# Optimization experiments

Hardware: AMD Instinct MI355X
Metric: run time of the kernel (lower is better)

The kernel has to match this reference:

```python
import jax, jax.numpy as jnp
import numpy as np

NEG_SLOPE = 0.01  # F.leaky_relu default

def setup_inputs() -> dict:
    key = jax.random.key(0)
    ks = jax.random.split(key, 5)
    N, in_dim, out_dim = 8192, 256, 256
    x = jax.random.normal(ks[0], (N, in_dim), dtype=jnp.float32)
    W_fc = jax.random.normal(ks[1], (in_dim, out_dim), dtype=jnp.float32) / np.sqrt(in_dim)
    b_fc = jnp.zeros((out_dim,), dtype=jnp.float32)
    # attn_fc weight [2*out_dim] split into the two halves acting on h_i and h_j
    a1 = jax.random.normal(ks[2], (out_dim,), dtype=jnp.float32) / np.sqrt(2 * out_dim)
    a2 = jax.random.normal(ks[3], (out_dim,), dtype=jnp.float32) / np.sqrt(2 * out_dim)
    a_b = jnp.zeros((), dtype=jnp.float32)
    return {"x": x, "W_fc": W_fc, "b_fc": b_fc, "a1": a1, "a2": a2, "a_b": a_b}

def reference(x, W_fc, b_fc, a1, a2, a_b):
    # h = fc(x)
    h = x @ W_fc + b_fc                       # [N, out_dim]
    # attn_fc(cat[h_i, h_j]) == h_i.a1 + h_j.a2 + a_b (exact decomposition of the Linear)
    s1 = h @ a1                               # [N]
    s2 = h @ a2                               # [N]
    e = jax.nn.leaky_relu(s1[:, None] + s2[None, :] + a_b, NEG_SLOPE)  # [N, N]
    attention = jax.nn.softmax(e, axis=1)     # row-softmax over neighbors j
    return attention @ h                      # [N, out_dim]
```

## Files before the change

### kernel.cpp

```cpp
#include <hip/hip_runtime.h>
#include <math.h>


#define NN 8192
#define DD 256
#define NB 8192
#define CH 512
#define POS (NN / CH)
#define RANGE 8.0f
#define SCALE (NB / (2.0f * RANGE))
#define NEG_SLOPE 0.01f

__device__ __forceinline__ int bucket_of(float v) {
    v = fminf(fmaxf(v, -RANGE), RANGE);
    int b = (int)floorf((v + RANGE) * SCALE);
    if (b < 0) b = 0;
    if (b > NB - 1) b = NB - 1;
    return b;
}

__global__ __launch_bounds__(256) void ka_gemm(
    const float* __restrict__ x, const float* __restrict__ W,
    const float* __restrict__ bfc, const float* __restrict__ a1,
    const float* __restrict__ a2,
    float* __restrict__ h, float* __restrict__ s1, float* __restrict__ s2,
    float* __restrict__ E, float* __restrict__ F, int* __restrict__ cnt)
{
    const int t = threadIdx.x;
    const int ct = t & 63;
    const int rt = t >> 6;
    const int row0 = blockIdx.x * 16;
    __shared__ float xs[16][DD];

#pragma unroll
    for (int i = 0; i < 4; ++i) {
        const int f = i * 256 + t;
        const int r = f >> 6, c4 = f & 63;
        *reinterpret_cast<float4*>(&xs[r][c4 * 4]) =
            *reinterpret_cast<const float4*>(&x[(size_t)(row0 + r) * DD + c4 * 4]);
    }
    __syncthreads();

    float acc[4][4];
#pragma unroll
    for (int r = 0; r < 4; ++r)
#pragma unroll
        for (int c = 0; c < 4; ++c) acc[r][c] = 0.f;

#pragma unroll 2
    for (int k4 = 0; k4 < DD / 4; ++k4) {
        float4 wv[4];
#pragma unroll
        for (int kk = 0; kk < 4; ++kk)
            wv[kk] = *reinterpret_cast<const float4*>(&W[(size_t)(k4 * 4 + kk) * DD + ct * 4]);
        float4 xr[4];
#pragma unroll
        for (int r = 0; r < 4; ++r)
            xr[r] = *reinterpret_cast<const float4*>(&xs[rt * 4 + r][k4 * 4]);
#pragma unroll
        for (int kk = 0; kk < 4; ++kk) {
#pragma unroll
            for (int r = 0; r < 4; ++r) {
                const float xv = (kk == 0) ? xr[r].x : (kk == 1) ? xr[r].y : (kk == 2) ? xr[r].z : xr[r].w;
                acc[r][0] = fmaf(xv, wv[kk].x, acc[r][0]);
                acc[r][1] = fmaf(xv, wv[kk].y, acc[r][1]);
                acc[r][2] = fmaf(xv, wv[kk].z, acc[r][2]);
                acc[r][3] = fmaf(xv, wv[kk].w, acc[r][3]);
            }
        }
    }

    const float4 bv  = *reinterpret_cast<const float4*>(&bfc[ct * 4]);
    const float4 a1v = *reinterpret_cast<const float4*>(&a1[ct * 4]);
    const float4 a2v = *reinterpret_cast<const float4*>(&a2[ct * 4]);
    const int lane = t & 63;

#pragma unroll
    for (int r = 0; r < 4; ++r) {
        acc[r][0] += bv.x; acc[r][1] += bv.y; acc[r][2] += bv.z; acc[r][3] += bv.w;
        const int row = row0 + rt * 4 + r;
        float4 hv = make_float4(acc[r][0], acc[r][1], acc[r][2], acc[r][3]);
        *reinterpret_cast<float4*>(&h[(size_t)row * DD + ct * 4]) = hv;
        float v1 = acc[r][0] * a1v.x + acc[r][1] * a1v.y + acc[r][2] * a1v.z + acc[r][3] * a1v.w;
        float v2 = acc[r][0] * a2v.x + acc[r][1] * a2v.y + acc[r][2] * a2v.z + acc[r][3] * a2v.w;
#pragma unroll
        for (int off = 32; off; off >>= 1) {
            v1 += __shfl_xor(v1, off, 64);
            v2 += __shfl_xor(v2, off, 64);
        }
        if (lane == 0) {
            s1[row] = v1;
            s2[row] = v2;
            E[row] = expf(v2);
            F[row] = expf(NEG_SLOPE * v2);
            atomicAdd(&cnt[bucket_of(v2)], 1);
        }
    }
}

__global__ __launch_bounds__(256) void kb_scan(int* __restrict__ cnt, int* __restrict__ boff)
{
    __shared__ int lds[256];
    const int t = threadIdx.x;
    const int base = t * 32;
    int loc[32];
    int s = 0;
#pragma unroll
    for (int k = 0; k < 32; ++k) { loc[k] = s; s += cnt[base + k]; }
    lds[t] = s;
    __syncthreads();
    for (int off = 1; off < 256; off <<= 1) {
        const int v = (t >= off) ? lds[t - off] : 0;
        __syncthreads();
        lds[t] += v;
        __syncthreads();
    }
    const int excl = (t > 0) ? lds[t - 1] : 0;
#pragma unroll
    for (int k = 0; k < 32; ++k) {
        const int val = excl + loc[k];
        boff[base + k] = val;
        cnt[base + k] = val;
    }
    if (t == 0) boff[NB] = NN;
}

__global__ __launch_bounds__(256) void kc_scatter(
    const float* __restrict__ s2, int* __restrict__ cursor, int* __restrict__ perm)
{
    const int j = blockIdx.x * blockDim.x + threadIdx.x;
    if (j < NN) {
        const int b = bucket_of(s2[j]);
        const int p = atomicAdd(&cursor[b], 1);
        perm[p] = j;
    }
}

__global__ __launch_bounds__(256) void kd1_tot(
    const float* __restrict__ h, const float* __restrict__ E, const float* __restrict__ F,
    const int* __restrict__ perm,
    float* __restrict__ TE, float* __restrict__ TF,
    float* __restrict__ sTE, float* __restrict__ sTF)
{
    const int c = blockIdx.x;
    const int t = threadIdx.x;
    __shared__ int jj[POS];
    __shared__ float Ee[POS], Ff[POS];
    if (t < POS) {
        const int j = perm[c * POS + t];
        jj[t] = j; Ee[t] = E[j]; Ff[t] = F[j];
    }
    __syncthreads();
    float te = 0.f, tf = 0.f;
#pragma unroll
    for (int k = 0; k < POS; ++k) {
        const float hv = h[(size_t)jj[k] * DD + t];
        te = fmaf(Ee[k], hv, te);
        tf = fmaf(Ff[k], hv, tf);
    }
    TE[c * DD + t] = te;
    TF[c * DD + t] = tf;
    if (t == 0) {
        float se = 0.f, sf = 0.f;
#pragma unroll
        for (int k = 0; k < POS; ++k) { se += Ee[k]; sf += Ff[k]; }
        sTE[c] = se; sTF[c] = sf;
    }
}

__global__ __launch_bounds__(512) void kd2_scan(
    float* __restrict__ TE, float* __restrict__ TF,
    float* __restrict__ sTE, float* __restrict__ sTF,
    float* __restrict__ PSE, float* __restrict__ PSF,
    float* __restrict__ psE, float* __restrict__ psF)
{
    const int t = threadIdx.x;
    const int b = blockIdx.x;
    __shared__ float lds[CH];

    if (b < 512) {
        const bool isE = (b < 256);
        const int d = isE ? b : (b - 256);
        float* __restrict__ A = isE ? TE : TF;
        const float v = A[(size_t)t * DD + d];
        const int pos = isE ? (CH - 1 - t) : t;
        lds[pos] = v;
        __syncthreads();
        for (int off = 1; off < CH; off <<= 1) {
            const float add = (pos >= off) ? lds[pos - off] : 0.f;
            __syncthreads();
            lds[pos] += add;
            __syncthreads();
        }
        const float incl = lds[pos];
        A[(size_t)t * DD + d] = incl - v;
        if (t == 0) {
            if (isE) PSE[(size_t)NN * DD + d] = 0.f;
            else     PSF[(size_t)NN * DD + d] = lds[CH - 1];
        }
    } else {
        const float vE = sTE[t];
        const float vF = sTF[t];
        lds[CH - 1 - t] = vE;
        __syncthreads();
        for (int off = 1; off < CH; off <<= 1) {
            const int pos = CH - 1 - t;
            const float add = (pos >= off) ? lds[pos - off] : 0.f;
            __syncthreads();
            lds[pos] += add;
            __syncthreads();
        }
        const float inclE = lds[CH - 1 - t];
        __syncthreads();
        lds[t] = vF;
        __syncthreads();
        for (int off = 1; off < CH; off <<= 1) {
            const float add = (t >= off) ? lds[t - off] : 0.f;
            __syncthreads();
            lds[t] += add;
            __syncthreads();
        }
        const float inclF = lds[t];
        const float totF = lds[CH - 1];
        sTE[t] = inclE - vE;
        sTF[t] = inclF - vF;
        if (t == 0) { psE[NN] = 0.f; psF[NN] = totF; }
    }
}

__global__ __launch_bounds__(256) void kd3_write(
    const float* __restrict__ h, const float* __restrict__ E, const float* __restrict__ F,
    const int* __restrict__ perm,
    const float* __restrict__ TE, const float* __restrict__ TF,
    const float* __restrict__ sTE, const float* __restrict__ sTF,
    float* __restrict__ PSE, float* __restrict__ PSF,
    float* __restrict__ psE, float* __restrict__ psF)
{
    const int c = blockIdx.x;
    const int t = threadIdx.x;
    __shared__ int jj[POS];
    __shared__ float Ee[POS], Ff[POS];
    if (t < POS) {
        const int j = perm[c * POS + t];
        jj[t] = j; Ee[t] = E[j]; Ff[t] = F[j];
    }
    __syncthreads();
    const int p0 = c * POS;

    float runE = TE[c * DD + t];
#pragma unroll
    for (int k = POS - 1; k >= 0; --k) {
        runE = fmaf(Ee[k], h[(size_t)jj[k] * DD + t], runE);
        PSE[(size_t)(p0 + k) * DD + t] = runE;
    }
    float runF = TF[c * DD + t];
#pragma unroll
    for (int k = 0; k < POS; ++k) {
        PSF[(size_t)(p0 + k) * DD + t] = runF;
        runF = fmaf(Ff[k], h[(size_t)jj[k] * DD + t], runF);
    }
    if (t == 0) {
        float rE = sTE[c];
#pragma unroll
        for (int k = POS - 1; k >= 0; --k) { rE += Ee[k]; psE[p0 + k] = rE; }
        float rF = sTF[c];
#pragma unroll
        for (int k = 0; k < POS; ++k) { psF[p0 + k] = rF; rF += Ff[k]; }
    }
}

__global__ __launch_bounds__(256) void ke_out(
    const float* __restrict__ h, const float* __restrict__ s1, const float* __restrict__ s2,
    const float* __restrict__ E, const float* __restrict__ F,
    const int* __restrict__ perm, const int* __restrict__ boff,
    const float* __restrict__ PSE, const float* __restrict__ PSF,
    const float* __restrict__ psE, const float* __restrict__ psF,
    const float* __restrict__ ab, float* __restrict__ out)
{
    const int i = blockIdx.x;
    const int t = threadIdx.x;
    const float c = s1[i] + ab[0];
    const float tau = -c;
    const int Bt = bucket_of(tau);
    const float A = expf(c);
    const float Alo = expf(NEG_SLOPE * c);

    const int p0 = boff[Bt], p1 = boff[Bt + 1];
    float num = A * PSE[(size_t)p1 * DD + t] + Alo * PSF[(size_t)p0 * DD + t];
    float den = A * psE[p1] + Alo * psF[p0];

    for (int p = p0; p < p1; ++p) {
        const int j = perm[p];
        const float hv = h[(size_t)j * DD + t];
        if (s2[j] >= tau) {
            const float w = A * E[j];
            num = fmaf(w, hv, num);
            den += w;
        } else {
            const float w = Alo * F[j];
            num = fmaf(w, hv, num);
            den += w;
        }
    }
    out[(size_t)i * DD + t] = num / den;
}

extern "C" void kernel_launch(void* const* d_in, const int* in_sizes, int n_in,
                              void* d_out, int out_size, void* d_ws, size_t ws_size,
                              hipStream_t stream)
{
    const float* x   = (const float*)d_in[0];
    const float* W   = (const float*)d_in[1];
    const float* bfc = (const float*)d_in[2];
    const float* a1  = (const float*)d_in[3];
    const float* a2  = (const float*)d_in[4];
    const float* ab  = (const float*)d_in[5];
    float* out = (float*)d_out;

    float* h   = (float*)d_ws;
    float* PSE = h + (size_t)NN * DD;
    float* PSF = PSE + (size_t)(NN + 1) * DD;
    float* TE  = PSF + (size_t)(NN + 1) * DD;
    float* TF  = TE + (size_t)CH * DD;
    float* s1  = TF + (size_t)CH * DD;
    float* s2  = s1 + NN;
    float* E   = s2 + NN;
    float* F   = E + NN;
    float* psE = F + NN;
    float* psF = psE + (NN + 1);
    float* sTE = psF + (NN + 1);
    float* sTF = sTE + CH;
    int* cnt   = (int*)(sTF + CH);
    int* boff  = cnt + NB;
    int* perm  = boff + (NB + 1);

    hipMemsetAsync(cnt, 0, NB * sizeof(int), stream);
    ka_gemm<<<NN / 16, 256, 0, stream>>>(x, W, bfc, a1, a2, h, s1, s2, E, F, cnt);
    kb_scan<<<1, 256, 0, stream>>>(cnt, boff);
    kc_scatter<<<NN / 256, 256, 0, stream>>>(s2, cnt, perm);
    kd1_tot<<<CH, 256, 0, stream>>>(h, E, F, perm, TE, TF, sTE, sTF);
    kd2_scan<<<513, 512, 0, stream>>>(TE, TF, sTE, sTF, PSE, PSF, psE, psF);
    kd3_write<<<CH, 256, 0, stream>>>(h, E, F, perm, TE, TF, sTE, sTF, PSE, PSF, psE, psF);
    ke_out<<<NN, 256, 0, stream>>>(h, s1, s2, E, F, perm, boff, PSE, PSF, psE, psF, ab, out);
}
```

Before: 144.2 us.

## Fully sort scores and replace per-position prefix arrays with chunk prefixes plus binary search

Adds a rank pass that fully sorts s2 within each bucket, so every row can binary-search its exact threshold position. The full N×D per-position prefix arrays PSE/PSF and their write kernel are removed. Each output row now combines a chunk-level prefix with a partial 16-element chunk walk, which cuts large memory writes and reads. Kernels are also reshaped to one wave per chunk or row with float4 loads, and exp is recomputed on the fly instead of stored. The trade-off is extra sequential work in the rank kernel when buckets are large, plus a per-row binary search.

```diff
diff --git a/kernel.cpp b/kernel.cpp
--- a/kernel.cpp
+++ b/kernel.cpp
@@ -24,7 +24,7 @@
     const float* __restrict__ bfc, const float* __restrict__ a1,
     const float* __restrict__ a2,
     float* __restrict__ h, float* __restrict__ s1, float* __restrict__ s2,
-    float* __restrict__ E, float* __restrict__ F, int* __restrict__ cnt)
+    int* __restrict__ cnt)
 {
     const int t = threadIdx.x;
     const int ct = t & 63;
@@ -91,8 +91,6 @@
         if (lane == 0) {
             s1[row] = v1;
             s2[row] = v2;
-            E[row] = expf(v2);
-            F[row] = expf(NEG_SLOPE * v2);
             atomicAdd(&cnt[bucket_of(v2)], 1);
         }
     }
@@ -136,173 +134,182 @@
     }
 }
 
+__global__ __launch_bounds__(256) void kc2_rank(
+    const float* __restrict__ s2, const int* __restrict__ perm,
+    const int* __restrict__ boff, int* __restrict__ perm2, float* __restrict__ s2s)
+{
+    const int j = blockIdx.x * blockDim.x + threadIdx.x;
+    if (j < NN) {
+        const float v = s2[j];
+        const int bk = bucket_of(v);
+        const int p0 = boff[bk], p1 = boff[bk + 1];
+        int rank = 0;
+        for (int p = p0; p < p1; ++p) {
+            const int k = perm[p];
+            const float vk = s2[k];
+            rank += (vk < v) || (vk == v && k < j);
+        }
+        const int pos = p0 + rank;
+        perm2[pos] = j;
+        s2s[pos] = v;
+    }
+}
+
 __global__ __launch_bounds__(256) void kd1_tot(
-    const float* __restrict__ h, const float* __restrict__ E, const float* __restrict__ F,
-    const int* __restrict__ perm,
+    const float* __restrict__ h, const int* __restrict__ perm2,
+    const float* __restrict__ s2s,
     float* __restrict__ TE, float* __restrict__ TF,
     float* __restrict__ sTE, float* __restrict__ sTF)
 {
-    const int c = blockIdx.x;
-    const int t = threadIdx.x;
-    __shared__ int jj[POS];
-    __shared__ float Ee[POS], Ff[POS];
-    if (t < POS) {
-        const int j = perm[c * POS + t];
-        jj[t] = j; Ee[t] = E[j]; Ff[t] = F[j];
-    }
+    const int w = threadIdx.x >> 6, lane = threadIdx.x & 63;
+    const int c = blockIdx.x * 4 + w;
+    const int p0 = c * POS;
+    float vE[POS], vF[POS];
+    int jj[POS];
+#pragma unroll
+    for (int k = 0; k < POS; ++k) {
+        const float v = s2s[p0 + k];
+        vE[k] = expf(v);
+        vF[k] = expf(NEG_SLOPE * v);
+        jj[k] = perm2[p0 + k];
+    }
+    float4 te = make_float4(0.f, 0.f, 0.f, 0.f);
+    float4 tf = make_float4(0.f, 0.f, 0.f, 0.f);
+#pragma unroll
+    for (int k = 0; k < POS; ++k) {
+        const float4 hv = *reinterpret_cast<const float4*>(&h[(size_t)jj[k] * DD + lane * 4]);
+        te.x = fmaf(vE[k], hv.x, te.x); te.y = fmaf(vE[k], hv.y, te.y);
+        te.z = fmaf(vE[k], hv.z, te.z); te.w = fmaf(vE[k], hv.w, te.w);
+        tf.x = fmaf(vF[k], hv.x, tf.x); tf.y = fmaf(vF[k], hv.y, tf.y);
+        tf.z = fmaf(vF[k], hv.z, tf.z); tf.w = fmaf(vF[k], hv.w, tf.w);
+    }
+    *reinterpret_cast<float4*>(&TE[(size_t)c * DD + lane * 4]) = te;
+    *reinterpret_cast<float4*>(&TF[(size_t)c * DD + lane * 4]) = tf;
+    if (lane == 0) {
+        float se = 0.f, sf = 0.f;
+#pragma unroll
+        for (int k = 0; k < POS; ++k) { se += vE[k]; sf += vF[k]; }
+        sTE[c] = se; sTF[c] = sf;
+    }
+}
+
+__device__ __forceinline__ void scan512_excl(float* lds, float* tmp, int t)
+{
+    const float a0 = lds[2 * t], a1 = lds[2 * t + 1];
+    tmp[t] = a0 + a1;
     __syncthreads();
-    float te = 0.f, tf = 0.f;
-#pragma unroll
-    for (int k = 0; k < POS; ++k) {
-        const float hv = h[(size_t)jj[k] * DD + t];
-        te = fmaf(Ee[k], hv, te);
-        tf = fmaf(Ff[k], hv, tf);
-    }
-    TE[c * DD + t] = te;
-    TF[c * DD + t] = tf;
-    if (t == 0) {
-        float se = 0.f, sf = 0.f;
-#pragma unroll
-        for (int k = 0; k < POS; ++k) { se += Ee[k]; sf += Ff[k]; }
-        sTE[c] = se; sTF[c] = sf;
-    }
-}
-
-__global__ __launch_bounds__(512) void kd2_scan(
+    for (int off = 1; off < 256; off <<= 1) {
+        const float v = (t >= off) ? tmp[t - off] : 0.f;
+        __syncthreads();
+        tmp[t] += v;
+        __syncthreads();
+    }
+    const float base = (t > 0) ? tmp[t - 1] : 0.f;
+    lds[2 * t] = base;
+    lds[2 * t + 1] = base + a0;
+    __syncthreads();
+}
+
+__global__ __launch_bounds__(256) void kd2_scan(
     float* __restrict__ TE, float* __restrict__ TF,
-    float* __restrict__ sTE, float* __restrict__ sTF,
-    float* __restrict__ PSE, float* __restrict__ PSF,
-    float* __restrict__ psE, float* __restrict__ psF)
+    float* __restrict__ sTE, float* __restrict__ sTF)
 {
     const int t = threadIdx.x;
     const int b = blockIdx.x;
     __shared__ float lds[CH];
-
-    if (b < 512) {
-        const bool isE = (b < 256);
-        const int d = isE ? b : (b - 256);
-        float* __restrict__ A = isE ? TE : TF;
-        const float v = A[(size_t)t * DD + d];
-        const int pos = isE ? (CH - 1 - t) : t;
-        lds[pos] = v;
-        __syncthreads();
-        for (int off = 1; off < CH; off <<= 1) {
-            const float add = (pos >= off) ? lds[pos - off] : 0.f;
-            __syncthreads();
-            lds[pos] += add;
-            __syncthreads();
-        }
-        const float incl = lds[pos];
-        A[(size_t)t * DD + d] = incl - v;
-        if (t == 0) {
-            if (isE) PSE[(size_t)NN * DD + d] = 0.f;
-            else     PSF[(size_t)NN * DD + d] = lds[CH - 1];
-        }
+    __shared__ float tmp[256];
+    const int q0 = 2 * t, q1 = 2 * t + 1;
+
+    if (b < 256) {
+        const int d = b;
+        lds[q0] = TE[(size_t)(511 - q0) * DD + d];
+        lds[q1] = TE[(size_t)(511 - q1) * DD + d];
+        __syncthreads();
+        scan512_excl(lds, tmp, t);
+        TE[(size_t)(511 - q0) * DD + d] = lds[q0];
+        TE[(size_t)(511 - q1) * DD + d] = lds[q1];
+        if (t == 0) TE[(size_t)CH * DD + d] = 0.f;
+    } else if (b < 512) {
+        const int d = b - 256;
+        lds[q0] = TF[(size_t)q0 * DD + d];
+        lds[q1] = TF[(size_t)q1 * DD + d];
+        __syncthreads();
+        scan512_excl(lds, tmp, t);
+        TF[(size_t)q0 * DD + d] = lds[q0];
+        TF[(size_t)q1 * DD + d] = lds[q1];
+        if (t == 0) TF[(size_t)CH * DD + d] = tmp[255];
     } else {
-        const float vE = sTE[t];
-        const float vF = sTF[t];
-        lds[CH - 1 - t] = vE;
-        __syncthreads();
-        for (int off = 1; off < CH; off <<= 1) {
-            const int pos = CH - 1 - t;
-            const float add = (pos >= off) ? lds[pos - off] : 0.f;
-            __syncthreads();
-            lds[pos] += add;
-            __syncthreads();
-        }
-        const float inclE = lds[CH - 1 - t];
-        __syncthreads();
-        lds[t] = vF;
-        __syncthreads();
-        for (int off = 1; off < CH; off <<= 1) {
-            const float add = (t >= off) ? lds[t - off] : 0.f;
-            __syncthreads();
-            lds[t] += add;
-            __syncthreads();
-        }
-        const float inclF = lds[t];
-        const float totF = lds[CH - 1];
-        sTE[t] = inclE - vE;
-        sTF[t] = inclF - vF;
-        if (t == 0) { psE[NN] = 0.f; psF[NN] = totF; }
-    }
-}
-
-__global__ __launch_bounds__(256) void kd3_write(
-    const float* __restrict__ h, const float* __restrict__ E, const float* __restrict__ F,
-    const int* __restrict__ perm,
+        lds[q0] = sTE[511 - q0]; lds[q1] = sTE[511 - q1];
+        __syncthreads();
+        scan512_excl(lds, tmp, t);
+        sTE[511 - q0] = lds[q0]; sTE[511 - q1] = lds[q1];
+        if (t == 0) sTE[CH] = 0.f;
+        __syncthreads();
+        lds[q0] = sTF[q0]; lds[q1] = sTF[q1];
+        __syncthreads();
+        scan512_excl(lds, tmp, t);
+        sTF[q0] = lds[q0]; sTF[q1] = lds[q1];
+        if (t == 0) sTF[CH] = tmp[255];
+    }
+}
+
+__global__ __launch_bounds__(256) void ke_out(
+    const float* __restrict__ h, const float* __restrict__ s1,
+    const float* __restrict__ s2s, const int* __restrict__ perm2,
     const float* __restrict__ TE, const float* __restrict__ TF,
     const float* __restrict__ sTE, const float* __restrict__ sTF,
-    float* __restrict__ PSE, float* __restrict__ PSF,
-    float* __restrict__ psE, float* __restrict__ psF)
-{
-    const int c = blockIdx.x;
-    const int t = threadIdx.x;
-    __shared__ int jj[POS];
-    __shared__ float Ee[POS], Ff[POS];
-    if (t < POS) {
-        const int j = perm[c * POS + t];
-        jj[t] = j; Ee[t] = E[j]; Ff[t] = F[j];
-    }
-    __syncthreads();
-    const int p0 = c * POS;
-
-    float runE = TE[c * DD + t];
-#pragma unroll
-    for (int k = POS - 1; k >= 0; --k) {
-        runE = fmaf(Ee[k], h[(size_t)jj[k] * DD + t], runE);
-        PSE[(size_t)(p0 + k) * DD + t] = runE;
-    }
-    float runF = TF[c * DD + t];
-#pragma unroll
-    for (int k = 0; k < POS; ++k) {
-        PSF[(size_t)(p0 + k) * DD + t] = runF;
-        runF = fmaf(Ff[k], h[(size_t)jj[k] * DD + t], runF);
-    }
-    if (t == 0) {
-        float rE = sTE[c];
-#pragma unroll
-        for (int k = POS - 1; k >= 0; --k) { rE += Ee[k]; psE[p0 + k] = rE; }
-        float rF = sTF[c];
-#pragma unroll
-        for (int k = 0; k < POS; ++k) { psF[p0 + k] = rF; rF += Ff[k]; }
-    }
-}
-
-__global__ __launch_bounds__(256) void ke_out(
-    const float* __restrict__ h, const float* __restrict__ s1, const float* __restrict__ s2,
-    const float* __restrict__ E, const float* __restrict__ F,
-    const int* __restrict__ perm, const int* __restrict__ boff,
-    const float* __restrict__ PSE, const float* __restrict__ PSF,
-    const float* __restrict__ psE, const float* __restrict__ psF,
     const float* __restrict__ ab, float* __restrict__ out)
 {
-    const int i = blockIdx.x;
-    const int t = threadIdx.x;
+    const int w = threadIdx.x >> 6, lane = threadIdx.x & 63;
+    const int i = blockIdx.x * 4 + w;
     const float c = s1[i] + ab[0];
     const float tau = -c;
-    const int Bt = bucket_of(tau);
     const float A = expf(c);
     const float Alo = expf(NEG_SLOPE * c);
 
-    const int p0 = boff[Bt], p1 = boff[Bt + 1];
-    float num = A * PSE[(size_t)p1 * DD + t] + Alo * PSF[(size_t)p0 * DD + t];
-    float den = A * psE[p1] + Alo * psF[p0];
-
-    for (int p = p0; p < p1; ++p) {
-        const int j = perm[p];
-        const float hv = h[(size_t)j * DD + t];
-        if (s2[j] >= tau) {
-            const float w = A * E[j];
-            num = fmaf(w, hv, num);
-            den += w;
-        } else {
-            const float w = Alo * F[j];
-            num = fmaf(w, hv, num);
-            den += w;
-        }
-    }
-    out[(size_t)i * DD + t] = num / den;
+    int lo = 0, hi = NN;
+    while (lo < hi) {
+        const int mid = (lo + hi) >> 1;
+        const bool lt = (s2s[mid] < tau);
+        lo = lt ? (mid + 1) : lo;
+        hi = lt ? hi : mid;
+    }
+    const int c0 = lo >> 4;
+    const int m = lo & 15;
+
+    float4 numE = *reinterpret_cast<const float4*>(&TE[(size_t)c0 * DD + lane * 4]);
+    float4 numF = *reinterpret_cast<const float4*>(&TF[(size_t)c0 * DD + lane * 4]);
+    float denE = sTE[c0];
+    float denF = sTF[c0];
+
+    if (c0 < CH) {
+        const int p0 = c0 * POS;
+#pragma unroll
+        for (int k = 0; k < POS; ++k) {
+            const float v = s2s[p0 + k];
+            const int j = perm2[p0 + k];
+            const float4 hv = *reinterpret_cast<const float4*>(&h[(size_t)j * DD + lane * 4]);
+            if (k >= m) {
+                const float e = expf(v);
+                numE.x = fmaf(e, hv.x, numE.x); numE.y = fmaf(e, hv.y, numE.y);
+                numE.z = fmaf(e, hv.z, numE.z); numE.w = fmaf(e, hv.w, numE.w);
+                denE += e;
+            } else {
+                const float f = expf(NEG_SLOPE * v);
+                numF.x = fmaf(f, hv.x, numF.x); numF.y = fmaf(f, hv.y, numF.y);
+                numF.z = fmaf(f, hv.z, numF.z); numF.w = fmaf(f, hv.w, numF.w);
+                denF += f;
+            }
+        }
+    }
+
+    const float inv = 1.f / fmaf(A, denE, Alo * denF);
+    float4 o;
+    o.x = fmaf(A, numE.x, Alo * numF.x) * inv;
+    o.y = fmaf(A, numE.y, Alo * numF.y) * inv;
+    o.z = fmaf(A, numE.z, Alo * numF.z) * inv;
+    o.w = fmaf(A, numE.w, Alo * numF.w) * inv;
+    *reinterpret_cast<float4*>(&out[(size_t)i * DD + lane * 4]) = o;
 }
 
 extern "C" void kernel_launch(void* const* d_in, const int* in_sizes, int n_in,
@@ -317,29 +324,25 @@
     const float* ab  = (const float*)d_in[5];
     float* out = (float*)d_out;
 
-    float* h   = (float*)d_ws;
-    float* PSE = h + (size_t)NN * DD;
-    float* PSF = PSE + (size_t)(NN + 1) * DD;
-    float* TE  = PSF + (size_t)(NN + 1) * DD;
-    float* TF  = TE + (size_t)CH * DD;
-    float* s1  = TF + (size_t)CH * DD;
-    float* s2  = s1 + NN;
-    float* E   = s2 + NN;
-    float* F   = E + NN;
-    float* psE = F + NN;
-    float* psF = psE + (NN + 1);
-    float* sTE = psF + (NN + 1);
-    float* sTF = sTE + CH;
-    int* cnt   = (int*)(sTF + CH);
-    int* boff  = cnt + NB;
-    int* perm  = boff + (NB + 1);
+    float* h    = (float*)d_ws;
+    float* TE   = h + (size_t)NN * DD;
+    float* TF   = TE + (size_t)(CH + 1) * DD;
+    float* s1   = TF + (size_t)(CH + 1) * DD;
+    float* s2   = s1 + NN;
+    float* s2s  = s2 + NN;
+    float* sTE  = s2s + NN;
+    float* sTF  = sTE + (CH + 1);
+    int* cnt    = (int*)(sTF + (CH + 1));
+    int* boff   = cnt + NB;
+    int* perm   = boff + (NB + 1);
+    int* perm2  = perm + NN;
 
     hipMemsetAsync(cnt, 0, NB * sizeof(int), stream);
-    ka_gemm<<<NN / 16, 256, 0, stream>>>(x, W, bfc, a1, a2, h, s1, s2, E, F, cnt);
-    kb_scan<<<1, 256, 0, stream>>>(cnt, boff);
+    ka_gemm <<<NN / 16, 256, 0, stream>>>(x, W, bfc, a1, a2, h, s1, s2, cnt);
+    kb_scan <<<1, 256, 0, stream>>>(cnt, boff);
     kc_scatter<<<NN / 256, 256, 0, stream>>>(s2, cnt, perm);
-    kd1_tot<<<CH, 256, 0, stream>>>(h, E, F, perm, TE, TF, sTE, sTF);
-    kd2_scan<<<513, 512, 0, stream>>>(TE, TF, sTE, sTF, PSE, PSF, psE, psF);
-    kd3_write<<<CH, 256, 0, stream>>>(h, E, F, perm, TE, TF, sTE, sTF, PSE, PSF, psE, psF);
-    ke_out<<<NN, 256, 0, stream>>>(h, s1, s2, E, F, perm, boff, PSE, PSF, psE, psF, ab, out);
-}
+    kc2_rank<<<NN / 256, 256, 0, stream>>>(s2, perm, boff, perm2, s2s);
+    kd1_tot <<<CH / 4, 256, 0, stream>>>(h, perm2, s2s, TE, TF, sTE, sTF);
+    kd2_scan<<<513, 256, 0, stream>>>(TE, TF, sTE, sTF);
+    ke_out  <<<NN / 4, 256, 0, stream>>>(h, s1, s2s, perm2, TE, TF, sTE, sTF, ab, out);
+}
```

Measured after the change: 142.9 us. Within noise of the previous version (-0.9%).
